# Optimization experiments

Measured on AMD Instinct MI355X. Metric: run time of the kernel, lower is better.

## Reference

```python
import jax, jax.numpy as jnp
import numpy as np

B, S, D = 2, 1024, 1024
N_HEADS = 16
R = 128
M = 8
N_NEURONS = 256


def group_gate(gate, n_basis):
    # gate: [B,S,N] -> [B,S,M], sum over consecutive groups, then normalize
    b, s, n = gate.shape
    gs = n // n_basis  # exact by construction (256/8)
    g = gate.reshape(b, s, n_basis, gs).sum(axis=-1)
    return g / (g.sum(axis=-1, keepdims=True) + 1e-8)


def feature_fn(x, neurons, weights):
    # x:[B,S,D], neurons:[M,D,R], weights:[B,S,M] -> h:[B,S,R]
    all_h = jnp.einsum('bsd,mdr->bsmr', x, neurons)
    return jnp.einsum('bsmr,bsm->bsr', all_h, weights)


def restore_fn(h, neurons, weights):
    # h:[B,S,R], neurons:[M,R,D], weights:[B,S,M] -> [B,S,D]
    pre = jnp.einsum('bsr,bsm->bsmr', h, weights)
    return jnp.einsum('bsmr,mrd->bsd', pre, neurons)


def setup_inputs() -> dict:
    key = jax.random.key(0)
    ks = jax.random.split(key, 9)
    sc = 0.02
    return {
        'x': jax.random.normal(ks[0], (B, S, D), jnp.float32),
        'qk_f': jax.random.normal(ks[1], (M, D, R), jnp.float32) * sc,
        'qk_r': jax.random.normal(ks[2], (M, R, D), jnp.float32) * sc,
        'v_f': jax.random.normal(ks[3], (M, D, R), jnp.float32) * sc,
        'v_r': jax.random.normal(ks[4], (M, R, D), jnp.float32) * sc,
        'Wg_q': jax.random.normal(ks[5], (D, N_NEURONS), jnp.float32) * sc,
        'Wg_k': jax.random.normal(ks[6], (D, N_NEURONS), jnp.float32) * sc,
        'Wg_v': jax.random.normal(ks[7], (D, N_NEURONS), jnp.float32) * sc,
        'W_O': jax.random.normal(ks[8], (D, D), jnp.float32) * sc,
    }


def reference(x, qk_f, qk_r, v_f, v_r, Wg_q, Wg_k, Wg_v, W_O):
    # Router gates (softmax over neuron dim), then grouped per basis
    g_Q = jax.nn.softmax(jnp.einsum('bsd,dn->bsn', x, Wg_q), axis=-1)
    g_K = jax.nn.softmax(jnp.einsum('bsd,dn->bsn', x, Wg_k), axis=-1)
    g_V = jax.nn.softmax(jnp.einsum('bsd,dn->bsn', x, Wg_v), axis=-1)
    gQ_b = group_gate(g_Q, M)
    gK_b = group_gate(g_K, M)
    gV_b = group_gate(g_V, M)

    Q = restore_fn(feature_fn(x, qk_f, gQ_b), qk_r, gQ_b)
    K = restore_fn(feature_fn(x, qk_f, gK_b), qk_r, gK_b)
    V = restore_fn(feature_fn(x, v_f, gV_b), v_r, gV_b)

    d_head = D // N_HEADS
    Q = Q.reshape(B, S, N_HEADS, d_head).transpose(0, 2, 1, 3)
    K = K.reshape(B, S, N_HEADS, d_head).transpose(0, 2, 1, 3)
    V = V.reshape(B, S, N_HEADS, d_head).transpose(0, 2, 1, 3)

    scale = jnp.sqrt(jnp.float32(d_head))
    scores = jnp.einsum('bhsd,bhtd->bhst', Q, K) / scale
    causal = jnp.tril(jnp.ones((S, S), dtype=jnp.bool_))
    scores = jnp.where(causal, scores, jnp.finfo(scores.dtype).min)
    attn_w = jax.nn.softmax(scores, axis=-1)
    out = jnp.einsum('bhst,bhtd->bhsd', attn_w, V)
    out = out.transpose(0, 2, 1, 3).reshape(B, S, D)
    out = jnp.einsum('bsd,de->bse', out, W_O)
    return out
```

## Files before the change

kernel.cpp:

```cpp
#include <hip/hip_runtime.h>
#include <hip/hip_bf16.h>

#define BB 2
#define SS 1024
#define DD 1024
#define NH 16
#define DH 64
#define MM 8
#define RR 128
#define NN 256
#define NT (BB*SS)

using bf16 = __hip_bfloat16;

typedef __attribute__((ext_vector_type(8))) short short8;
typedef __attribute__((ext_vector_type(4))) short short4v;
typedef __attribute__((ext_vector_type(4))) float f32x4;

#define EXP2F(x) __builtin_amdgcn_exp2f(x)

#define GLD16(g, l) __builtin_amdgcn_global_load_lds( \
    (const __attribute__((address_space(1))) void*)(g), \
    (__attribute__((address_space(3))) void*)(l), 16, 0, 0)

__device__ __forceinline__ short8 lds_load8(const short* p) {
    short4v a = *(const short4v*)p;
    short4v b = *(const short4v*)(p + 4);
    short8 r;
    r[0] = a[0]; r[1] = a[1]; r[2] = a[2]; r[3] = a[3];
    r[4] = b[0]; r[5] = b[1]; r[6] = b[2]; r[7] = b[3];
    return r;
}

template <int NR>
__device__ __forceinline__ void stage_tile(const bf16* __restrict__ src, int k0,
                                           bf16* lds, int wave, int lane) {
#pragma unroll
    for (int i = 0; i < NR / 32; ++i) {
        const int L = i * 256 + wave * 64 + lane;
        const int row = L >> 3;
        const int gch = (L & 7) ^ ((row >> 1) & 7);
        GLD16(src + (size_t)row * DD + k0 + gch * 8, &lds[(i * 256 + wave * 64) * 8]);
    }
}

__device__ __forceinline__ short8 fragld(const bf16* lds, int rc, int kk, int quad) {
    int slot = (kk * 4 + quad) ^ ((rc >> 1) & 7);
    return *(const short8*)&((const short*)lds)[(rc * 8 + slot) * 8];
}

__device__ __forceinline__ void gemm64_pipe2(
    const bf16* __restrict__ A, const bf16* __restrict__ Bt, bf16* __restrict__ C,
    int Nz, int m0, int n0, bf16* As, bf16* Bs,
    int wave, int lane, int quad, int l15) {
    const int wr = wave >> 1, wc = wave & 1;
    f32x4 acc[2][4];
#pragma unroll
    for (int i = 0; i < 2; ++i)
#pragma unroll
        for (int j = 0; j < 4; ++j) acc[i][j] = (f32x4)0.f;

    const bf16* Ab = A + (size_t)m0 * DD;
    const bf16* Bb = Bt + (size_t)n0 * DD;

    stage_tile<64>(Ab, 0, As, wave, lane);
    stage_tile<128>(Bb, 0, Bs, wave, lane);
    stage_tile<64>(Ab, 64, As + 4096, wave, lane);
    stage_tile<128>(Bb, 64, Bs + 8192, wave, lane);

    int cur = 0;
    for (int it = 0; it < 16; ++it) {
        const int k0 = it * 64;
        int nxt = cur + 2; if (nxt >= 3) nxt -= 3;
        if (it < 14) {
            stage_tile<64>(Ab, k0 + 128, As + nxt * 4096, wave, lane);
            stage_tile<128>(Bb, k0 + 128, Bs + nxt * 8192, wave, lane);
            asm volatile("s_waitcnt vmcnt(12)" ::: "memory");
        } else if (it == 14) {
            asm volatile("s_waitcnt vmcnt(6)" ::: "memory");
        } else {
            asm volatile("s_waitcnt vmcnt(0)" ::: "memory");
        }
        __builtin_amdgcn_s_barrier();

        const bf16* Asc = As + cur * 4096;
        const bf16* Bsc = Bs + cur * 8192;
#pragma unroll
        for (int kk = 0; kk < 2; ++kk) {
            short8 aF[2], bF[4];
#pragma unroll
            for (int bi = 0; bi < 2; ++bi) aF[bi] = fragld(Asc, wr * 32 + bi * 16 + l15, kk, quad);
#pragma unroll
            for (int bj = 0; bj < 4; ++bj) bF[bj] = fragld(Bsc, wc * 64 + bj * 16 + l15, kk, quad);
#pragma unroll
            for (int bi = 0; bi < 2; ++bi)
#pragma unroll
                for (int bj = 0; bj < 4; ++bj)
                    acc[bi][bj] = __builtin_amdgcn_mfma_f32_16x16x32_bf16(aF[bi], bF[bj], acc[bi][bj], 0, 0, 0);
        }
        __builtin_amdgcn_s_barrier();
        cur = cur + 1; if (cur == 3) cur = 0;
    }

#pragma unroll
    for (int bi = 0; bi < 2; ++bi)
#pragma unroll
        for (int bj = 0; bj < 4; ++bj)
#pragma unroll
            for (int r = 0; r < 4; ++r) {
                int row = m0 + wr * 32 + bi * 16 + quad * 4 + r;
                int col = n0 + wc * 64 + bj * 16 + l15;
                C[(size_t)row * Nz + col] = __float2bfloat16(acc[bi][bj][r]);
            }
}

struct ProjArgs {
    const bf16 *xb, *f0, *f1, *wg;
    bf16 *allh0, *allh1, *lg;
    const float* csrc[3];
    bf16* cdst[3];
};

__global__ __launch_bounds__(256, 2) void mfma_proj(ProjArgs P) {
    __shared__ __align__(16) char smem[73728];
    const int bidx = blockIdx.x;
    const int tid = threadIdx.x;

    if (bidx >= 704) {
        float (*tile)[33] = (float(*)[33])smem;
        const int cb = bidx - 704;
        const int j = cb >> 10;
        const int t = cb & 1023;
        const int kb = t >> 5, rb = t & 31;
        const int tx = tid & 31, ty0 = tid >> 5;
        const float* s = P.csrc[j] + ((size_t)(kb * 32) * 1024) + rb * 32 + tx;
#pragma unroll
        for (int p = 0; p < 4; ++p)
            tile[ty0 + p * 8][tx] = s[(size_t)(ty0 + p * 8) * 1024];
        __syncthreads();
        bf16* dd = P.cdst[j] + ((size_t)(rb * 32) * 1024) + kb * 32 + tx;
#pragma unroll
        for (int p = 0; p < 4; ++p)
            dd[(size_t)(ty0 + p * 8) * 1024] = __float2bfloat16(tile[tx][ty0 + p * 8]);
        return;
    }

    bf16* As = (bf16*)smem;
    bf16* Bs = As + 3 * 64 * 64;
    const int wave = tid >> 6, lane = tid & 63;
    const int quad = lane >> 4, l15 = lane & 15;
    const int wk = (bidx & 7) * 88 + (bidx >> 3);
    if (wk < 512) {
        const int z = wk >> 8;
        const int r = wk & 255;
        gemm64_pipe2(P.xb, z ? P.f1 : P.f0, z ? P.allh1 : P.allh0, 1024,
                     (r >> 3) * 64, (r & 7) * 128, As, Bs, wave, lane, quad, l15);
    } else {
        const int r = wk - 512;
        gemm64_pipe2(P.xb, P.wg, P.lg, 768, (r / 6) * 64, (r % 6) * 128,
                     As, Bs, wave, lane, quad, l15);
    }
}

struct RestZ {
    const bf16* A[3];
    const bf16* Bt[3];
    bf16* C[3];
};

__global__ __launch_bounds__(256, 2) void mfma_restore(RestZ R) {
    __shared__ __align__(16) char smem[73728];
    bf16* As = (bf16*)smem;
    bf16* Bs = As + 3 * 64 * 64;
    const int tid = threadIdx.x;
    const int wave = tid >> 6, lane = tid & 63;
    const int quad = lane >> 4, l15 = lane & 15;
    const int wk = (blockIdx.x & 7) * 96 + (blockIdx.x >> 3);
    const int z = wk >> 8;
    const int r = wk & 255;
    gemm64_pipe2(R.A[z], R.Bt[z], R.C[z], DD, (r >> 3) * 64, (r & 7) * 128,
                 As, Bs, wave, lane, quad, l15);
}

__global__ __launch_bounds__(256, 3) void mfma_wo(
    const bf16* __restrict__ A, const bf16* __restrict__ Bt, float* __restrict__ C) {
    __shared__ __align__(16) bf16 As[3 * 64 * 64];
    __shared__ __align__(16) bf16 Bs[3 * 64 * 64];
    const int tid = threadIdx.x;
    const int wave = tid >> 6, lane = tid & 63;
    const int quad = lane >> 4, l15 = lane & 15;
    const int wr = wave >> 1, wc = wave & 1;
    const int wk = (blockIdx.x & 7) * 64 + (blockIdx.x >> 3);
    const int m0 = (wk >> 4) * 64, n0 = (wk & 15) * 64;

    f32x4 acc[2][2];
#pragma unroll
    for (int i = 0; i < 2; ++i)
#pragma unroll
        for (int j = 0; j < 2; ++j) acc[i][j] = (f32x4)0.f;

    const bf16* Ab = A + (size_t)m0 * DD;
    const bf16* Bb = Bt + (size_t)n0 * DD;

    stage_tile<64>(Ab, 0, As, wave, lane);
    stage_tile<64>(Bb, 0, Bs, wave, lane);
    stage_tile<64>(Ab, 64, As + 4096, wave, lane);
    stage_tile<64>(Bb, 64, Bs + 4096, wave, lane);

    int cur = 0;
    for (int it = 0; it < 16; ++it) {
        const int k0 = it * 64;
        int nxt = cur + 2; if (nxt >= 3) nxt -= 3;
        if (it < 14) {
            stage_tile<64>(Ab, k0 + 128, As + nxt * 4096, wave, lane);
            stage_tile<64>(Bb, k0 + 128, Bs + nxt * 4096, wave, lane);
            asm volatile("s_waitcnt vmcnt(8)" ::: "memory");
        } else if (it == 14) {
            asm volatile("s_waitcnt vmcnt(4)" ::: "memory");
        } else {
            asm volatile("s_waitcnt vmcnt(0)" ::: "memory");
        }
        __builtin_amdgcn_s_barrier();

        const bf16* Asc = As + cur * 4096;
        const bf16* Bsc = Bs + cur * 4096;
#pragma unroll
        for (int kk = 0; kk < 2; ++kk) {
            short8 aF[2], bF[2];
#pragma unroll
            for (int bi = 0; bi < 2; ++bi) aF[bi] = fragld(Asc, wr * 32 + bi * 16 + l15, kk, quad);
#pragma unroll
            for (int bj = 0; bj < 2; ++bj) bF[bj] = fragld(Bsc, wc * 32 + bj * 16 + l15, kk, quad);
#pragma unroll
            for (int bi = 0; bi < 2; ++bi)
#pragma unroll
                for (int bj = 0; bj < 2; ++bj)
                    acc[bi][bj] = __builtin_amdgcn_mfma_f32_16x16x32_bf16(aF[bi], bF[bj], acc[bi][bj], 0, 0, 0);
        }
        __builtin_amdgcn_s_barrier();
        cur = cur + 1; if (cur == 3) cur = 0;
    }
#pragma unroll
    for (int bi = 0; bi < 2; ++bi)
#pragma unroll
        for (int bj = 0; bj < 2; ++bj)
#pragma unroll
            for (int r = 0; r < 4; ++r) {
                int row = m0 + wr * 32 + bi * 16 + quad * 4 + r;
                int col = n0 + wc * 32 + bj * 16 + l15;
                C[(size_t)row * DD + col] = acc[bi][bj][r];
            }
}

struct ConvJobs {
    const float* src[9];
    bf16* dst[9];
    int K[9], R[9], G[9];
    int tEnd[9];
};

__global__ void convert_kernel(ConvJobs J) {
    __shared__ float tile[32][33];
    const int b = blockIdx.x;
    int j = 0;
    while (j < 8 && b >= J.tEnd[j]) ++j;
    const int local = b - (j > 0 ? J.tEnd[j - 1] : 0);
    const float* src = J.src[j];
    bf16* dst = J.dst[j];
    const int tid = threadIdx.x;

    if (J.G[j] == 0) {
        size_t base = (size_t)local * 4096 + (size_t)tid * 16;
        const float4* s4 = (const float4*)(src + base);
        short* d = (short*)(dst + base);
#pragma unroll
        for (int c = 0; c < 4; ++c) {
            float4 v = s4[c];
            short4v o;
            bf16 t0 = __float2bfloat16(v.x); o[0] = *(short*)&t0;
            bf16 t1 = __float2bfloat16(v.y); o[1] = *(short*)&t1;
            bf16 t2 = __float2bfloat16(v.z); o[2] = *(short*)&t2;
            bf16 t3 = __float2bfloat16(v.w); o[3] = *(short*)&t3;
            *(short4v*)(d + c * 4) = o;
        }
    } else {
        const int Kj = J.K[j], Rj = J.R[j];
        const int Rb = Rj >> 5, Kb = Kj >> 5;
        const int perG = Kb * Rb;
        const int g = local / perG;
        const int rem = local - g * perG;
        const int kb = rem / Rb, rb = rem - kb * Rb;
        const int tx = tid & 31, ty0 = tid >> 5;
        const float* s = src + ((size_t)(g * Kj + kb * 32) * Rj) + rb * 32 + tx;
#pragma unroll
        for (int p = 0; p < 4; ++p)
            tile[ty0 + p * 8][tx] = s[(size_t)(ty0 + p * 8) * Rj];
        __syncthreads();
        bf16* dd = dst + ((size_t)(g * Rj + rb * 32) * Kj) + kb * 32 + tx;
#pragma unroll
        for (int p = 0; p < 4; ++p)
            dd[(size_t)(ty0 + p * 8) * Kj] = __float2bfloat16(tile[tx][ty0 + p * 8]);
    }
}

__global__ void gate_combine(const bf16* __restrict__ logitsAll,
                             const bf16* __restrict__ allh,
                             bf16* __restrict__ preQ, bf16* __restrict__ preK,
                             bf16* __restrict__ preV) {
    const int t = blockIdx.x;
    const int n = threadIdx.x;
    const int wave = n >> 6, lane = n & 63;
    __shared__ float wred[3][4];
    __shared__ float sred[3][4];
    __shared__ float gred[3][8];

    float v[3], e[3];
#pragma unroll
    for (int z = 0; z < 3; ++z)
        v[z] = __bfloat162float(logitsAll[(size_t)t * 768 + z * 256 + n]);

    float mz[3];
#pragma unroll
    for (int z = 0; z < 3; ++z) {
        mz[z] = v[z];
#pragma unroll
        for (int off = 1; off <= 32; off <<= 1)
            mz[z] = fmaxf(mz[z], __shfl_xor(mz[z], off));
    }
    if (lane == 0) {
#pragma unroll
        for (int z = 0; z < 3; ++z) wred[z][wave] = mz[z];
    }
    __syncthreads();
    float gmax[3];
#pragma unroll
    for (int z = 0; z < 3; ++z)
        gmax[z] = fmaxf(fmaxf(wred[z][0], wred[z][1]), fmaxf(wred[z][2], wred[z][3]));

    float ws[3];
#pragma unroll
    for (int z = 0; z < 3; ++z) {
        e[z] = __expf(v[z] - gmax[z]);
        ws[z] = e[z];
#pragma unroll
        for (int off = 1; off <= 32; off <<= 1)
            ws[z] += __shfl_xor(ws[z], off);
    }
    if (lane == 0) {
#pragma unroll
        for (int z = 0; z < 3; ++z) sred[z][wave] = ws[z];
    }
    float gs[3];
#pragma unroll
    for (int z = 0; z < 3; ++z) {
        gs[z] = e[z];
#pragma unroll
        for (int off = 1; off <= 16; off <<= 1)
            gs[z] += __shfl_xor(gs[z], off);
    }
    __syncthreads();
    float total[3];
#pragma unroll
    for (int z = 0; z < 3; ++z)
        total[z] = sred[z][0] + sred[z][1] + sred[z][2] + sred[z][3];
    if ((n & 31) == 0) {
#pragma unroll
        for (int z = 0; z < 3; ++z) gred[z][n >> 5] = gs[z] / total[z];
    }
    __syncthreads();

    float gv[3][8];
#pragma unroll
    for (int z = 0; z < 3; ++z) {
        float tot = 0.f;
#pragma unroll
        for (int m = 0; m < 8; ++m) tot += gred[z][m];
        float inv = 1.0f / (tot + 1e-8f);
#pragma unroll
        for (int m = 0; m < 8; ++m) gv[z][m] = gred[z][m] * inv;
    }

    const int r0 = n & 127;
    const int half = n >> 7;
    const bf16* src_qk = allh + (size_t)t * 1024;
    const bf16* src_v  = allh + (size_t)NT * DD + (size_t)t * 1024;
    float hq = 0.f, hk = 0.f, hv = 0.f;
#pragma unroll
    for (int m = 0; m < 8; ++m) {
        float aqk = __bfloat162float(src_qk[m * 128 + r0]);
        float av  = __bfloat162float(src_v[m * 128 + r0]);
        hq += aqk * gv[0][m];
        hk += aqk * gv[1][m];
        hv += av  * gv[2][m];
    }
    __syncthreads();
#pragma unroll
    for (int mm = 0; mm < 4; ++mm) {
        int m = half * 4 + mm;
        size_t o = (size_t)t * 1024 + m * 128 + r0;
        preQ[o] = __float2bfloat16(hq * gv[0][m]);
        preK[o] = __float2bfloat16(hk * gv[1][m]);
        preV[o] = __float2bfloat16(hv * gv[2][m]);
    }
}

#define LDK 68

__global__ __launch_bounds__(256) void flash_attn_causal(
    const bf16* __restrict__ Q, const bf16* __restrict__ K,
    const bf16* __restrict__ V, bf16* __restrict__ out) {
    const int bx = blockIdx.x;
    const int xcd = bx & 7, slot = bx >> 3;
    const int bh = xcd * 4 + (slot & 3);
    const int qtk = slot >> 2;
    const int qt = (qtk < 8) ? (15 - qtk) : (qtk - 8);
    const int b = bh >> 4;
    const int h = bh & 15;
    const int kt_hi = qt + 1;

    const int tid = threadIdx.x;
    const int wave = tid >> 6;
    const int lane = tid & 63;
    const int quad = lane >> 4;
    const int l15 = lane & 15;

    __shared__ short Ks[2][64 * 64];
    __shared__ short Vt[2][64 * LDK];
    __shared__ short Ps[4 * 16 * LDK];

    const int q_row = qt * 64 + wave * 16 + l15;
    const bf16* qptr = Q + (size_t)(b * SS + q_row) * DD + h * DH + quad * 8;
    short8 aq0 = *(const short8*)qptr;
    short8 aq1 = *(const short8*)(qptr + 32);

    const int krp = tid & 31;
    const int dhb = (tid >> 5) * 8;

    float m_r[4], l_r[4];
    f32x4 o[4];
#pragma unroll
    for (int r = 0; r < 4; ++r) { m_r[r] = -3.0e38f; l_r[r] = 0.f; }
#pragma unroll
    for (int cc = 0; cc < 4; ++cc) o[cc] = (f32x4)0.f;

    const float SCL2 = 0.18033688f;

    {
#pragma unroll
        for (int i = 0; i < 2; ++i) {
            const int L = i * 256 + wave * 64 + lane;
            const int row = L >> 3;
            const int gch = (L & 7) ^ ((row >> 1) & 7);
            GLD16(K + (size_t)(b * SS + row) * DD + h * DH + gch * 8,
                  &Ks[0][(i * 256 + wave * 64) * 8]);
        }
        const bf16* s0 = V + (size_t)(b * SS + 2 * krp) * DD + h * DH + dhb;
        short8 r0 = *(const short8*)s0;
        short8 r1 = *(const short8*)(s0 + DD);
#pragma unroll
        for (int i = 0; i < 8; ++i) {
            unsigned int pk = (unsigned short)r0[i] | ((unsigned int)(unsigned short)r1[i] << 16);
            *(unsigned int*)&Vt[0][(dhb + i) * LDK + 2 * krp] = pk;
        }
        __syncthreads();
    }

    for (int kt = 0; kt < kt_hi; ++kt) {
        const int buf = kt & 1;
        const bool pf = (kt + 1 < kt_hi);
        short8 pr0, pr1;
        if (pf) {
#pragma unroll
            for (int i = 0; i < 2; ++i) {
                const int L = i * 256 + wave * 64 + lane;
                const int row = L >> 3;
                const int gch = (L & 7) ^ ((row >> 1) & 7);
                GLD16(K + (size_t)(b * SS + (kt + 1) * 64 + row) * DD + h * DH + gch * 8,
                      &Ks[buf ^ 1][(i * 256 + wave * 64) * 8]);
            }
            const bf16* s0 = V + (size_t)(b * SS + (kt + 1) * 64 + 2 * krp) * DD + h * DH + dhb;
            pr0 = *(const short8*)s0;
            pr1 = *(const short8*)(s0 + DD);
        }

        const short* KsB = Ks[buf];
        f32x4 s[4];
#pragma unroll
        for (int cc = 0; cc < 4; ++cc) {
            int n = cc * 16 + l15;
            int sl0 = quad ^ ((n >> 1) & 7);
            int sl1 = (quad + 4) ^ ((n >> 1) & 7);
            short8 bk0 = *(const short8*)&KsB[(n * 8 + sl0) * 8];
            short8 bk1 = *(const short8*)&KsB[(n * 8 + sl1) * 8];
            f32x4 acc = (f32x4)0.f;
            acc = __builtin_amdgcn_mfma_f32_16x16x32_bf16(aq0, bk0, acc, 0, 0, 0);
            acc = __builtin_amdgcn_mfma_f32_16x16x32_bf16(aq1, bk1, acc, 0, 0, 0);
            s[cc] = acc;
        }

        const bool diag = (kt == qt);
#pragma unroll
        for (int cc = 0; cc < 4; ++cc) {
#pragma unroll
            for (int r = 0; r < 4; ++r) {
                float v = s[cc][r] * SCL2;
                if (diag) {
                    int row_rel = wave * 16 + quad * 4 + r;
                    int col_rel = cc * 16 + l15;
                    if (col_rel > row_rel) v = -3.0e38f;
                }
                s[cc][r] = v;
            }
        }

        float mx[4];
#pragma unroll
        for (int r = 0; r < 4; ++r) {
            float m2 = fmaxf(fmaxf(s[0][r], s[1][r]), fmaxf(s[2][r], s[3][r]));
            m2 = fmaxf(m2, __shfl_xor(m2, 1));
            m2 = fmaxf(m2, __shfl_xor(m2, 2));
            m2 = fmaxf(m2, __shfl_xor(m2, 4));
            m2 = fmaxf(m2, __shfl_xor(m2, 8));
            mx[r] = m2;
        }
        bool grew = false;
#pragma unroll
        for (int r = 0; r < 4; ++r) grew = grew || (mx[r] > m_r[r] + 8.f);
        float alpha[4];
        const bool need = __any(grew);
        if (need) {
#pragma unroll
            for (int r = 0; r < 4; ++r) {
                float nm = fmaxf(m_r[r], mx[r]);
                alpha[r] = EXP2F(m_r[r] - nm);
                m_r[r] = nm;
            }
        }

        float p[4][4];
#pragma unroll
        for (int r = 0; r < 4; ++r) {
            float rs = 0.f;
#pragma unroll
            for (int cc = 0; cc < 4; ++cc) {
                float e = EXP2F(s[cc][r] - m_r[r]);
                p[cc][r] = e;
                rs += e;
            }
            rs += __shfl_xor(rs, 1);
            rs += __shfl_xor(rs, 2);
            rs += __shfl_xor(rs, 4);
            rs += __shfl_xor(rs, 8);
            if (need) l_r[r] = l_r[r] * alpha[r] + rs;
            else      l_r[r] += rs;
        }
        if (need) {
#pragma unroll
            for (int cc = 0; cc < 4; ++cc)
#pragma unroll
                for (int r = 0; r < 4; ++r) o[cc][r] *= alpha[r];
        }

        short* pw = &Ps[wave * 16 * LDK];
#pragma unroll
        for (int cc = 0; cc < 4; ++cc)
#pragma unroll
            for (int r = 0; r < 4; ++r) {
                bf16 hb = __float2bfloat16(p[cc][r]);
                pw[(quad * 4 + r) * LDK + cc * 16 + l15] = *(short*)&hb;
            }

        short8 ap0 = lds_load8(&pw[l15 * LDK + quad * 8]);
        short8 ap1 = lds_load8(&pw[l15 * LDK + 32 + quad * 8]);

        const short* VtB = Vt[buf];
#pragma unroll
        for (int cc = 0; cc < 4; ++cc) {
            short8 bv0 = lds_load8(&VtB[(cc * 16 + l15) * LDK + quad * 8]);
            short8 bv1 = lds_load8(&VtB[(cc * 16 + l15) * LDK + 32 + quad * 8]);
            o[cc] = __builtin_amdgcn_mfma_f32_16x16x32_bf16(ap0, bv0, o[cc], 0, 0, 0);
            o[cc] = __builtin_amdgcn_mfma_f32_16x16x32_bf16(ap1, bv1, o[cc], 0, 0, 0);
        }

        if (pf) {
#pragma unroll
            for (int i = 0; i < 8; ++i) {
                unsigned int pk = (unsigned short)pr0[i] | ((unsigned int)(unsigned short)pr1[i] << 16);
                *(unsigned int*)&Vt[buf ^ 1][(dhb + i) * LDK + 2 * krp] = pk;
            }
        }
        __syncthreads();
    }

    float inv[4];
#pragma unroll
    for (int r = 0; r < 4; ++r) inv[r] = 1.0f / l_r[r];
#pragma unroll
    for (int cc = 0; cc < 4; ++cc)
#pragma unroll
        for (int r = 0; r < 4; ++r) {
            int row = qt * 64 + wave * 16 + quad * 4 + r;
            out[(size_t)(b * SS + row) * DD + h * DH + cc * 16 + l15] =
                __float2bfloat16(o[cc][r] * inv[r]);
        }
}

extern "C" void kernel_launch(void* const* d_in, const int* in_sizes, int n_in,
                              void* d_out, int out_size, void* d_ws, size_t ws_size,
                              hipStream_t stream) {
    const float* x    = (const float*)d_in[0];
    const float* qk_f = (const float*)d_in[1];
    const float* qk_r = (const float*)d_in[2];
    const float* v_f  = (const float*)d_in[3];
    const float* v_r  = (const float*)d_in[4];
    const float* Wg_q = (const float*)d_in[5];
    const float* Wg_k = (const float*)d_in[6];
    const float* Wg_v = (const float*)d_in[7];
    const float* W_O  = (const float*)d_in[8];

    char* w = (char*)d_ws;
    const size_t MB = 1 << 20;
    bf16* xb     = (bf16*)(w + 0);
    bf16* wg_bt  = (bf16*)(w + 4 * MB);
    bf16* fbt    = (bf16*)(w + (size_t)(5.5 * MB));
    bf16* logits = (bf16*)(w + (size_t)(9.5 * MB));
    bf16* qkr_bt = (bf16*)(w + 16 * MB);
    bf16* vr_bt  = (bf16*)(w + 18 * MB);
    bf16* wo_bt  = (bf16*)(w + 20 * MB);
    bf16* preQ   = (bf16*)(w + 0);
    bf16* preK   = (bf16*)(w + 4 * MB);
    bf16* Kb     = (bf16*)(w + 8 * MB);
    bf16* Vb     = (bf16*)(w + 12 * MB);
    bf16* attnb  = (bf16*)(w + 0);
    bf16* allh   = (bf16*)d_out;
    bf16* preV   = allh + (size_t)NT * DD;
    bf16* Qb     = (bf16*)d_out;
    float* out   = (float*)d_out;

    ConvJobs J;
    J.src[0] = x;    J.dst[0] = xb;               J.K[0] = 0;    J.R[0] = 0;    J.G[0] = 0;
    J.src[1] = qk_f; J.dst[1] = fbt;              J.K[1] = 1024; J.R[1] = 128;  J.G[1] = 8;
    J.src[2] = v_f;  J.dst[2] = fbt + 1024*1024;  J.K[2] = 1024; J.R[2] = 128;  J.G[2] = 8;
    J.src[3] = Wg_q; J.dst[3] = wg_bt;            J.K[3] = 1024; J.R[3] = 256;  J.G[3] = 1;
    J.src[4] = Wg_k; J.dst[4] = wg_bt + 256*1024; J.K[4] = 1024; J.R[4] = 256;  J.G[4] = 1;
    J.src[5] = Wg_v; J.dst[5] = wg_bt + 2*256*1024; J.K[5] = 1024; J.R[5] = 256; J.G[5] = 1;
    int tiles[6] = {512, 1024, 1024, 256, 256, 256};
    int cum = 0;
    for (int i = 0; i < 6; ++i) { cum += tiles[i]; J.tEnd[i] = cum; }
    for (int i = 6; i < 9; ++i) { J.tEnd[i] = cum; J.src[i] = nullptr; J.dst[i] = nullptr; J.K[i] = J.R[i] = J.G[i] = 0; }
    convert_kernel<<<cum, 256, 0, stream>>>(J);

    ProjArgs Pp;
    Pp.xb = xb; Pp.f0 = fbt; Pp.f1 = fbt + 1024*1024; Pp.wg = wg_bt;
    Pp.allh0 = allh; Pp.allh1 = allh + (size_t)NT * DD; Pp.lg = logits;
    Pp.csrc[0] = qk_r; Pp.csrc[1] = v_r; Pp.csrc[2] = W_O;
    Pp.cdst[0] = qkr_bt; Pp.cdst[1] = vr_bt; Pp.cdst[2] = wo_bt;
    mfma_proj<<<dim3(3776), 256, 0, stream>>>(Pp);

    gate_combine<<<NT, 256, 0, stream>>>(logits, allh, preQ, preK, preV);

    RestZ Pr;
    Pr.A[0] = preQ; Pr.A[1] = preK; Pr.A[2] = preV;
    Pr.Bt[0] = qkr_bt; Pr.Bt[1] = qkr_bt; Pr.Bt[2] = vr_bt;
    Pr.C[0] = Qb; Pr.C[1] = Kb; Pr.C[2] = Vb;
    mfma_restore<<<dim3(768), 256, 0, stream>>>(Pr);

    flash_attn_causal<<<dim3(512), 256, 0, stream>>>(Qb, Kb, Vb, attnb);

    mfma_wo<<<dim3(512), 256, 0, stream>>>(attnb, wo_bt, out);
}
```

Measured before the change: 183.0 us.

## Split long causal query tiles across two blocks and merge with a combine kernel

Query tiles 8-15 of the causal flash attention now have their key range split into two halves, each handled by a separate block. The blocks write unnormalized fp32 partial outputs plus per-row max and sum to workspace, and a new combine kernel merges them into bf16. A lookup table orders the work so the heaviest items are scheduled first. The aim is to balance load across CUs and shorten the tail, at the cost of an extra launch and extra fp32 partial traffic.

Measured after the change: 179.2 us. 1.02x faster.

```diff
diff --git a/kernel.cpp b/kernel.cpp
--- a/kernel.cpp
+++ b/kernel.cpp
@@ -406,17 +406,30 @@
 
 #define LDK 68
 
-__global__ __launch_bounds__(256) void flash_attn_causal(
+__device__ const int FW24[24] = {
+    62, 63, 60, 61, 14,
+    58, 59, 56, 12,
+    57, 54, 55, 52, 10,
+    53, 50, 51, 48, 8,
+    49, 6,
+    4, 2, 0
+};
+
+__global__ __launch_bounds__(256) void flash_attn_hybrid(
     const bf16* __restrict__ Q, const bf16* __restrict__ K,
-    const bf16* __restrict__ V, bf16* __restrict__ out) {
+    const bf16* __restrict__ V, bf16* __restrict__ out,
+    float* __restrict__ Opart, float* __restrict__ ml) {
     const int bx = blockIdx.x;
-    const int xcd = bx & 7, slot = bx >> 3;
-    const int bh = xcd * 4 + (slot & 3);
-    const int qtk = slot >> 2;
-    const int qt = (qtk < 8) ? (15 - qtk) : (qtk - 8);
+    const int e = FW24[bx >> 5];
+    const int bh = bx & 31;
+    const int split = e >> 5;
+    const int qt = (e >> 1) & 15;
+    const int half = e & 1;
+    const int h0 = (qt + 2) >> 1;
+    const int kt_lo = (split && half) ? h0 : 0;
+    const int kt_hi = (split && !half) ? h0 : (qt + 1);
     const int b = bh >> 4;
     const int h = bh & 15;
-    const int kt_hi = qt + 1;
 
     const int tid = threadIdx.x;
     const int wave = tid >> 6;
@@ -451,10 +464,10 @@
             const int L = i * 256 + wave * 64 + lane;
             const int row = L >> 3;
             const int gch = (L & 7) ^ ((row >> 1) & 7);
-            GLD16(K + (size_t)(b * SS + row) * DD + h * DH + gch * 8,
+            GLD16(K + (size_t)(b * SS + kt_lo * 64 + row) * DD + h * DH + gch * 8,
                   &Ks[0][(i * 256 + wave * 64) * 8]);
         }
-        const bf16* s0 = V + (size_t)(b * SS + 2 * krp) * DD + h * DH + dhb;
+        const bf16* s0 = V + (size_t)(b * SS + kt_lo * 64 + 2 * krp) * DD + h * DH + dhb;
         short8 r0 = *(const short8*)s0;
         short8 r1 = *(const short8*)(s0 + DD);
 #pragma unroll
@@ -465,8 +478,8 @@
         __syncthreads();
     }
 
-    for (int kt = 0; kt < kt_hi; ++kt) {
-        const int buf = kt & 1;
+    for (int kt = kt_lo; kt < kt_hi; ++kt) {
+        const int buf = (kt - kt_lo) & 1;
         const bool pf = (kt + 1 < kt_hi);
         short8 pr0, pr1;
         if (pf) {
@@ -543,9 +556,9 @@
             float rs = 0.f;
 #pragma unroll
             for (int cc = 0; cc < 4; ++cc) {
-                float e = EXP2F(s[cc][r] - m_r[r]);
-                p[cc][r] = e;
-                rs += e;
+                float e2 = EXP2F(s[cc][r] - m_r[r]);
+                p[cc][r] = e2;
+                rs += e2;
             }
             rs += __shfl_xor(rs, 1);
             rs += __shfl_xor(rs, 2);
@@ -592,17 +605,74 @@
         __syncthreads();
     }
 
-    float inv[4];
-#pragma unroll
-    for (int r = 0; r < 4; ++r) inv[r] = 1.0f / l_r[r];
-#pragma unroll
-    for (int cc = 0; cc < 4; ++cc)
-#pragma unroll
-        for (int r = 0; r < 4; ++r) {
-            int row = qt * 64 + wave * 16 + quad * 4 + r;
-            out[(size_t)(b * SS + row) * DD + h * DH + cc * 16 + l15] =
-                __float2bfloat16(o[cc][r] * inv[r]);
-        }
+    if (!split) {
+        float inv[4];
+#pragma unroll
+        for (int r = 0; r < 4; ++r) inv[r] = 1.0f / l_r[r];
+#pragma unroll
+        for (int cc = 0; cc < 4; ++cc)
+#pragma unroll
+            for (int r = 0; r < 4; ++r) {
+                int row = qt * 64 + wave * 16 + quad * 4 + r;
+                out[(size_t)(b * SS + row) * DD + h * DH + cc * 16 + l15] =
+                    __float2bfloat16(o[cc][r] * inv[r]);
+            }
+    } else {
+        const int idx = (bh * 8 + (qt - 8)) * 2 + half;
+        float* ob = Opart + (size_t)idx * 4096;
+#pragma unroll
+        for (int cc = 0; cc < 4; ++cc)
+#pragma unroll
+            for (int r = 0; r < 4; ++r) {
+                int row = wave * 16 + quad * 4 + r;
+                ob[row * 64 + cc * 16 + l15] = o[cc][r];
+            }
+        if (l15 == 0) {
+#pragma unroll
+            for (int r = 0; r < 4; ++r) {
+                int row = wave * 16 + quad * 4 + r;
+                ml[(size_t)idx * 128 + row] = m_r[r];
+                ml[(size_t)idx * 128 + 64 + row] = l_r[r];
+            }
+        }
+    }
+}
+
+__global__ void attn_combine(const float* __restrict__ Opart,
+                             const float* __restrict__ ml,
+                             bf16* __restrict__ out) {
+    const int bidx = blockIdx.x;
+    const int bh = bidx & 31;
+    const int qt = (bidx >> 5) + 8;
+    const int b = bh >> 4;
+    const int h = bh & 15;
+    const int tid = threadIdx.x;
+    const int row = tid >> 2;
+    const int cg = tid & 3;
+
+    const int p0 = (bh * 8 + (qt - 8)) * 2;
+    const int p1 = p0 + 1;
+    float m0 = ml[(size_t)p0 * 128 + row], l0 = ml[(size_t)p0 * 128 + 64 + row];
+    float m1 = ml[(size_t)p1 * 128 + row], l1 = ml[(size_t)p1 * 128 + 64 + row];
+    float ms = fmaxf(m0, m1);
+    float w0 = EXP2F(m0 - ms), w1 = EXP2F(m1 - ms);
+    float inv = 1.0f / (l0 * w0 + l1 * w1);
+
+    const float* o0 = Opart + (size_t)p0 * 4096 + row * 64 + cg * 16;
+    const float* o1 = Opart + (size_t)p1 * 4096 + row * 64 + cg * 16;
+    short out16[16];
+#pragma unroll
+    for (int j = 0; j < 16; j += 4) {
+        float4 a = *(const float4*)(o0 + j);
+        float4 bb = *(const float4*)(o1 + j);
+        bf16 t0 = __float2bfloat16((a.x * w0 + bb.x * w1) * inv); out16[j] = *(short*)&t0;
+        bf16 t1 = __float2bfloat16((a.y * w0 + bb.y * w1) * inv); out16[j + 1] = *(short*)&t1;
+        bf16 t2 = __float2bfloat16((a.z * w0 + bb.z * w1) * inv); out16[j + 2] = *(short*)&t2;
+        bf16 t3 = __float2bfloat16((a.w * w0 + bb.w * w1) * inv); out16[j + 3] = *(short*)&t3;
+    }
+    short* dst = (short*)(out + (size_t)(b * SS + qt * 64 + row) * DD + h * DH + cg * 16);
+    *(short8*)dst = *(short8*)&out16[0];
+    *(short8*)(dst + 8) = *(short8*)&out16[8];
 }
 
 extern "C" void kernel_launch(void* const* d_in, const int* in_sizes, int n_in,
@@ -632,6 +702,8 @@
     bf16* Kb     = (bf16*)(w + 8 * MB);
     bf16* Vb     = (bf16*)(w + 12 * MB);
     bf16* attnb  = (bf16*)(w + 0);
+    float* Opart = (float*)(w + 32 * MB);
+    float* mlbuf = (float*)(w + 48 * MB);
     bf16* allh   = (bf16*)d_out;
     bf16* preV   = allh + (size_t)NT * DD;
     bf16* Qb     = (bf16*)d_out;
@@ -665,7 +737,9 @@
     Pr.C[0] = Qb; Pr.C[1] = Kb; Pr.C[2] = Vb;
     mfma_restore<<<dim3(768), 256, 0, stream>>>(Pr);
 
-    flash_attn_causal<<<dim3(512), 256, 0, stream>>>(Qb, Kb, Vb, attnb);
+    flash_attn_hybrid<<<dim3(768), 256, 0, stream>>>(Qb, Kb, Vb, attnb, Opart, mlbuf);
+
+    attn_combine<<<dim3(256), 256, 0, stream>>>(Opart, mlbuf, attnb);
 
     mfma_wo<<<dim3(512), 256, 0, stream>>>(attnb, wo_bt, out);
 }
```
